# Performance work log

Measured on AMD Instinct MI355X. Metric: run time of the kernel, lower is better.

Reference implementation:

```python
import jax, jax.numpy as jnp
import numpy as np

HIDDEN = 1024
HEADS = 16
N, T1, T2 = 2, 2048, 2048


def setup_inputs() -> dict:
    key = jax.random.key(0)
    k1, k2, k3, k4 = jax.random.split(key, 4)
    q = jax.random.normal(k1, (N, T1, HIDDEN), dtype=jnp.float32)
    encoder_k = jax.random.normal(k2, (N, T2, HIDDEN), dtype=jnp.float32)
    encoder_v = jax.random.normal(k3, (N, T2, HIDDEN), dtype=jnp.float32)
    encoder_attention_mask = jnp.zeros((N, 1, T2, T2), dtype=jnp.float32)
    wo_w = jax.random.normal(k4, (HIDDEN, HIDDEN), dtype=jnp.float32) * (1.0 / np.sqrt(HIDDEN))
    wo_b = jnp.zeros((HIDDEN,), dtype=jnp.float32)
    return {"q": q, "encoder_k": encoder_k, "encoder_v": encoder_v,
            "encoder_attention_mask": encoder_attention_mask,
            "wo_w": wo_w, "wo_b": wo_b}


def _split_heads(x):
    # [N, T, E] -> [N, h, T, d]
    n, t, e = x.shape
    return x.reshape(n, t, HEADS, e // HEADS).transpose(0, 2, 1, 3)


def reference(q, encoder_k, encoder_v, encoder_attention_mask, wo_w, wo_b):
    qh = _split_heads(q)            # [N,h,T1,d]
    kh = _split_heads(encoder_k)    # [N,h,T2,d]
    vh = _split_heads(encoder_v)    # [N,h,T2,d]
    # NOTE: original applies no 1/sqrt(d) scaling
    scores = jnp.einsum('bhqd,bhkd->bhqk', qh, kh) + encoder_attention_mask
    weights = jax.nn.softmax(scores, axis=-1)
    ctx = jnp.einsum('bhqk,bhkd->bhqd', weights, vh)   # [N,h,T1,d]
    ctx = ctx.transpose(0, 2, 1, 3).reshape(q.shape[0], q.shape[1], -1)  # [N,T1,E]
    # wo: Linear (torch: x @ W.T + b) followed by ReLU
    return jax.nn.relu(ctx @ wo_w.T + wo_b)
```

## Files before the change

kernel.cpp:

```cpp
#include <hip/hip_runtime.h>
#include <hip/hip_bf16.h>


typedef short short8 __attribute__((ext_vector_type(8)));
typedef short short4v __attribute__((ext_vector_type(4)));
typedef float floatx4 __attribute__((ext_vector_type(4)));

#define HIDDEN 1024
#define HEADS 16
#define NB 2
#define T1 2048
#define T2 2048

#define LOG2E 1.44269504f
#define SHIFT 28.8539004f
#define VS 68

__device__ __forceinline__ unsigned short f2bf(float f) {
    unsigned u = __float_as_uint(f);
    return (unsigned short)((u + 0x7fffu + ((u >> 16) & 1u)) >> 16);
}

__device__ __forceinline__ short f2bf_native(float f) {
    __hip_bfloat16 h = __float2bfloat16(f);
    return __builtin_bit_cast(short, h);
}

__global__ void zero_kernel(unsigned* f) {
    if (threadIdx.x == 0) *f = 0u;
}

__global__ void prep_kernel(const float4* __restrict__ ek, const float4* __restrict__ ev,
                            const float4* __restrict__ ww, const float4* __restrict__ mask,
                            ushort4* __restrict__ dst, unsigned* __restrict__ flag) {
    const int NK = NB * T2 * HIDDEN / 4;
    const int NW = HIDDEN * HIDDEN / 4;
    if (blockIdx.y == 0) {
        int i = blockIdx.x * blockDim.x + threadIdx.x;
        int stride = gridDim.x * blockDim.x;
        const int n = 2 * NK + NW;
        for (; i < n; i += stride) {
            float4 v = (i < NK) ? ek[i] : (i < 2 * NK) ? ev[i - NK] : ww[i - 2 * NK];
            ushort4 o;
            o.x = f2bf(v.x); o.y = f2bf(v.y); o.z = f2bf(v.z); o.w = f2bf(v.w);
            dst[i] = o;
        }
    } else {
        const int NM = NB * T2 * T2 / 4;
        int i = blockIdx.x * blockDim.x + threadIdx.x;
        int stride = gridDim.x * blockDim.x;
        float mx = 0.f;
        for (; i < NM; i += stride) {
            float4 v = mask[i];
            mx = fmaxf(mx, fmaxf(fmaxf(fabsf(v.x), fabsf(v.y)), fmaxf(fabsf(v.z), fabsf(v.w))));
        }
        for (int d = 32; d; d >>= 1) mx = fmaxf(mx, __shfl_xor(mx, d));
        if ((threadIdx.x & 63) == 0 && mx > 0.f) atomicMax(flag, __float_as_uint(mx));
    }
}

__device__ __forceinline__ void stage_v(short* __restrict__ buf, const short* __restrict__ Vb,
                                        int b, int h, int kc, int tid) {
#pragma unroll
    for (int it = 0; it < 2; ++it) {
        int i = tid + (it << 8);
        int key = i & 63, dg = i >> 6;
        short8 s = *(const short8*)&Vb[(((b * T2) + kc + key) << 10) + (h << 6) + (dg << 3)];
#pragma unroll
        for (int j = 0; j < 8; ++j) buf[(dg * 8 + j) * VS + key] = s[j];
    }
}

__global__ __launch_bounds__(256, 2) void attn_kernel(
        const float* __restrict__ q,
        const short* __restrict__ Kb,
        const short* __restrict__ Vb,
        const float* __restrict__ mask,
        const unsigned* __restrict__ flagp,
        short* __restrict__ ctx)
{
    __shared__ short lV[2][2][64 * VS];

    const int tid = threadIdx.x;
    const int wave = tid >> 6;
    const int lane = tid & 63;
    const int quad = lane >> 4;
    const int l16 = lane & 15;

    const int b = blockIdx.z;
    const int h = blockIdx.y;
    const int q0 = blockIdx.x * 128;

    const bool use_mask = (*flagp != 0u);

    short8 qf[2][2];
#pragma unroll
    for (int rb = 0; rb < 2; ++rb) {
#pragma unroll
        for (int ks = 0; ks < 2; ++ks) {
            const float* qp = q + (((b * T1) + q0 + wave * 32 + rb * 16 + l16) << 10)
                                + (h << 6) + ks * 32 + quad * 8;
            float4 v0 = *(const float4*)qp;
            float4 v1 = *(const float4*)(qp + 4);
            short8 s;
            s[0] = (short)f2bf(v0.x * LOG2E); s[1] = (short)f2bf(v0.y * LOG2E);
            s[2] = (short)f2bf(v0.z * LOG2E); s[3] = (short)f2bf(v0.w * LOG2E);
            s[4] = (short)f2bf(v1.x * LOG2E); s[5] = (short)f2bf(v1.y * LOG2E);
            s[6] = (short)f2bf(v1.z * LOG2E); s[7] = (short)f2bf(v1.w * LOG2E);
            qf[rb][ks] = s;
        }
    }

    floatx4 o_acc[2][4];
#pragma unroll
    for (int rb = 0; rb < 2; ++rb)
#pragma unroll
        for (int cb = 0; cb < 4; ++cb) o_acc[rb][cb] = (floatx4){0.f, 0.f, 0.f, 0.f};
    float l_st[2] = {0.f, 0.f};

    stage_v(lV[0][0], Vb, b, h, 0, tid);
    stage_v(lV[0][1], Vb, b, h, 64, tid);
    short8 kfrag[4][2];
#pragma unroll
    for (int kb = 0; kb < 4; ++kb)
#pragma unroll
        for (int ks = 0; ks < 2; ++ks)
            kfrag[kb][ks] = *(const short8*)
                &Kb[(((b * T2) + kb * 16 + l16) << 10) + (h << 6) + ks * 32 + quad * 8];
    __syncthreads();

    for (int icc = 0; icc < T2 / 128; ++icc) {
        const int kc0 = icc << 7;
        const bool has_next = (icc + 1 < T2 / 128);
        const int kcn = has_next ? kc0 + 128 : kc0;

        short8 vreg[4];
#pragma unroll
        for (int it = 0; it < 4; ++it) {
            int i = tid + ((it & 1) << 8);
            int key = i & 63, dg = i >> 6;
            int half = it >> 1;
            vreg[it] = *(const short8*)
                &Vb[(((b * T2) + kcn + half * 64 + key) << 10) + (h << 6) + (dg << 3)];
        }

        short8 knext[4][2];
#pragma unroll
        for (int kb = 0; kb < 4; ++kb)
#pragma unroll
            for (int ks = 0; ks < 2; ++ks)
                knext[kb][ks] = *(const short8*)
                    &Kb[(((b * T2) + kc0 + 64 + kb * 16 + l16) << 10) + (h << 6) + ks * 32 + quad * 8];

        {
            const short* cur = lV[icc & 1][0];
            const int kc = kc0;
            short4v vfrag[4][4];
#pragma unroll
            for (int kb = 0; kb < 4; ++kb)
#pragma unroll
                for (int cb = 0; cb < 4; ++cb)
                    vfrag[kb][cb] = *(const short4v*)&cur[(cb * 16 + l16) * VS + kb * 16 + quad * 4];

#pragma unroll
            for (int rb = 0; rb < 2; ++rb) {
                floatx4 st[4];
#pragma unroll
                for (int kb = 0; kb < 4; ++kb) {
                    floatx4 a = (floatx4){0.f, 0.f, 0.f, 0.f};
                    a = __builtin_amdgcn_mfma_f32_16x16x32_bf16(kfrag[kb][0], qf[rb][0], a, 0, 0, 0);
                    a = __builtin_amdgcn_mfma_f32_16x16x32_bf16(kfrag[kb][1], qf[rb][1], a, 0, 0, 0);
                    st[kb] = a;
                }
                if (use_mask) {
                    int qrow = q0 + wave * 32 + rb * 16 + l16;
#pragma unroll
                    for (int kb = 0; kb < 4; ++kb)
#pragma unroll
                        for (int r = 0; r < 4; ++r) {
                            int key = kc + kb * 16 + quad * 4 + r;
                            st[kb][r] += mask[(b * T2 + qrow) * T2 + key] * LOG2E;
                        }
                }
                float rs = 0.f;
                short4v pf[4];
#pragma unroll
                for (int kb = 0; kb < 4; ++kb) {
                    float p0 = exp2f(st[kb][0] - SHIFT);
                    float p1 = exp2f(st[kb][1] - SHIFT);
                    float p2 = exp2f(st[kb][2] - SHIFT);
                    float p3 = exp2f(st[kb][3] - SHIFT);
                    rs += (p0 + p1) + (p2 + p3);
                    pf[kb][0] = f2bf_native(p0);
                    pf[kb][1] = f2bf_native(p1);
                    pf[kb][2] = f2bf_native(p2);
                    pf[kb][3] = f2bf_native(p3);
                }
                rs += __shfl_xor(rs, 16);
                rs += __shfl_xor(rs, 32);
                l_st[rb] += rs;

#pragma unroll
                for (int kb = 0; kb < 4; ++kb)
#pragma unroll
                    for (int cb = 0; cb < 4; ++cb)
                        o_acc[rb][cb] = __builtin_amdgcn_mfma_f32_16x16x16bf16_1k(
                            vfrag[kb][cb], pf[kb], o_acc[rb][cb], 0, 0, 0);
            }
        }

#pragma unroll
        for (int kb = 0; kb < 4; ++kb)
#pragma unroll
            for (int ks = 0; ks < 2; ++ks)
                kfrag[kb][ks] = knext[kb][ks];

#pragma unroll
        for (int kb = 0; kb < 4; ++kb)
#pragma unroll
            for (int ks = 0; ks < 2; ++ks)
                knext[kb][ks] = *(const short8*)
                    &Kb[(((b * T2) + kcn + kb * 16 + l16) << 10) + (h << 6) + ks * 32 + quad * 8];

        {
            const short* cur = lV[icc & 1][1];
            const int kc = kc0 + 64;
            short4v vfrag[4][4];
#pragma unroll
            for (int kb = 0; kb < 4; ++kb)
#pragma unroll
                for (int cb = 0; cb < 4; ++cb)
                    vfrag[kb][cb] = *(const short4v*)&cur[(cb * 16 + l16) * VS + kb * 16 + quad * 4];

#pragma unroll
            for (int rb = 0; rb < 2; ++rb) {
                floatx4 st[4];
#pragma unroll
                for (int kb = 0; kb < 4; ++kb) {
                    floatx4 a = (floatx4){0.f, 0.f, 0.f, 0.f};
                    a = __builtin_amdgcn_mfma_f32_16x16x32_bf16(kfrag[kb][0], qf[rb][0], a, 0, 0, 0);
                    a = __builtin_amdgcn_mfma_f32_16x16x32_bf16(kfrag[kb][1], qf[rb][1], a, 0, 0, 0);
                    st[kb] = a;
                }
                if (use_mask) {
                    int qrow = q0 + wave * 32 + rb * 16 + l16;
#pragma unroll
                    for (int kb = 0; kb < 4; ++kb)
#pragma unroll
                        for (int r = 0; r < 4; ++r) {
                            int key = kc + kb * 16 + quad * 4 + r;
                            st[kb][r] += mask[(b * T2 + qrow) * T2 + key] * LOG2E;
                        }
                }
                float rs = 0.f;
                short4v pf[4];
#pragma unroll
                for (int kb = 0; kb < 4; ++kb) {
                    float p0 = exp2f(st[kb][0] - SHIFT);
                    float p1 = exp2f(st[kb][1] - SHIFT);
                    float p2 = exp2f(st[kb][2] - SHIFT);
                    float p3 = exp2f(st[kb][3] - SHIFT);
                    rs += (p0 + p1) + (p2 + p3);
                    pf[kb][0] = f2bf_native(p0);
                    pf[kb][1] = f2bf_native(p1);
                    pf[kb][2] = f2bf_native(p2);
                    pf[kb][3] = f2bf_native(p3);
                }
                rs += __shfl_xor(rs, 16);
                rs += __shfl_xor(rs, 32);
                l_st[rb] += rs;

#pragma unroll
                for (int kb = 0; kb < 4; ++kb)
#pragma unroll
                    for (int cb = 0; cb < 4; ++cb)
                        o_acc[rb][cb] = __builtin_amdgcn_mfma_f32_16x16x16bf16_1k(
                            vfrag[kb][cb], pf[kb], o_acc[rb][cb], 0, 0, 0);
            }
        }

#pragma unroll
        for (int kb = 0; kb < 4; ++kb)
#pragma unroll
            for (int ks = 0; ks < 2; ++ks)
                kfrag[kb][ks] = knext[kb][ks];

        if (has_next) {
#pragma unroll
            for (int it = 0; it < 4; ++it) {
                int i = tid + ((it & 1) << 8);
                int key = i & 63, dg = i >> 6;
                short* nbuf = lV[(icc + 1) & 1][it >> 1];
#pragma unroll
                for (int j = 0; j < 8; ++j) nbuf[(dg * 8 + j) * VS + key] = vreg[it][j];
            }
        }
        __syncthreads();
    }

#pragma unroll
    for (int rb = 0; rb < 2; ++rb) {
        float rinv = 1.0f / l_st[rb];
        int qrow = q0 + wave * 32 + rb * 16 + l16;
#pragma unroll
        for (int cb = 0; cb < 4; ++cb) {
            short4v o;
#pragma unroll
            for (int r = 0; r < 4; ++r) o[r] = (short)f2bf(o_acc[rb][cb][r] * rinv);
            *(short4v*)&ctx[((b * T1 + qrow) << 10) + (h << 6) + cb * 16 + quad * 4] = o;
        }
    }
}

__global__ __launch_bounds__(512) void proj_kernel(
        const short* __restrict__ Cb,
        const short* __restrict__ Wb,
        const float* __restrict__ bias,
        float* __restrict__ out)
{
    __shared__ short lA[2][64 * 72];
    __shared__ short lB[2][128 * 72];

    const int tid = threadIdx.x;
    const int wave = tid >> 6;
    const int lane = tid & 63;
    const int quad = lane >> 4;
    const int l16 = lane & 15;
    const int wm = wave >> 2, wn = wave & 3;
    const int bm = blockIdx.x, bn = blockIdx.y;

    floatx4 acc[2][2];
#pragma unroll
    for (int i = 0; i < 2; ++i)
#pragma unroll
        for (int j = 0; j < 2; ++j) acc[i][j] = (floatx4){0.f, 0.f, 0.f, 0.f};

    short8 ra, rbw[2];
    {
        int row = tid >> 3, c = tid & 7;
        ra = *(const short8*)&Cb[((bm * 64 + row) << 10) + c * 8];
#pragma unroll
        for (int it = 0; it < 2; ++it) {
            int i = tid + it * 512;
            int brow = i >> 3, bc = i & 7;
            rbw[it] = *(const short8*)&Wb[((bn * 128 + brow) << 10) + bc * 8];
        }
    }
    {
        int row = tid >> 3, c = tid & 7;
        *(short8*)&lA[0][row * 72 + c * 8] = ra;
#pragma unroll
        for (int it = 0; it < 2; ++it) {
            int i = tid + it * 512;
            int brow = i >> 3, bc = i & 7;
            *(short8*)&lB[0][brow * 72 + bc * 8] = rbw[it];
        }
    }
    __syncthreads();

    int cur = 0;
    for (int kt = 0; kt < 1024; kt += 64) {
        const bool has_next = (kt + 64 < 1024);
        if (has_next) {
            int row = tid >> 3, c = tid & 7;
            ra = *(const short8*)&Cb[((bm * 64 + row) << 10) + kt + 64 + c * 8];
#pragma unroll
            for (int it = 0; it < 2; ++it) {
                int i = tid + it * 512;
                int brow = i >> 3, bc = i & 7;
                rbw[it] = *(const short8*)&Wb[((bn * 128 + brow) << 10) + kt + 64 + bc * 8];
            }
        }

#pragma unroll
        for (int ks = 0; ks < 2; ++ks) {
            short8 af[2], bf[2];
#pragma unroll
            for (int i = 0; i < 2; ++i)
                af[i] = *(const short8*)&lA[cur][(wm * 32 + i * 16 + l16) * 72 + ks * 32 + quad * 8];
#pragma unroll
            for (int j = 0; j < 2; ++j)
                bf[j] = *(const short8*)&lB[cur][(wn * 32 + j * 16 + l16) * 72 + ks * 32 + quad * 8];
#pragma unroll
            for (int i = 0; i < 2; ++i)
#pragma unroll
                for (int j = 0; j < 2; ++j)
                    acc[i][j] = __builtin_amdgcn_mfma_f32_16x16x32_bf16(af[i], bf[j], acc[i][j], 0, 0, 0);
        }

        if (has_next) {
            int row = tid >> 3, c = tid & 7;
            *(short8*)&lA[cur ^ 1][row * 72 + c * 8] = ra;
#pragma unroll
            for (int it = 0; it < 2; ++it) {
                int i = tid + it * 512;
                int brow = i >> 3, bc = i & 7;
                *(short8*)&lB[cur ^ 1][brow * 72 + bc * 8] = rbw[it];
            }
        }
        __syncthreads();
        cur ^= 1;
    }

    float bv[2];
#pragma unroll
    for (int j = 0; j < 2; ++j) bv[j] = bias[bn * 128 + wn * 32 + j * 16 + l16];

#pragma unroll
    for (int i = 0; i < 2; ++i)
#pragma unroll
        for (int j = 0; j < 2; ++j)
#pragma unroll
            for (int r = 0; r < 4; ++r) {
                int row = bm * 64 + wm * 32 + i * 16 + quad * 4 + r;
                int col = bn * 128 + wn * 32 + j * 16 + l16;
                float v = acc[i][j][r] + bv[j];
                out[(row << 10) + col] = fmaxf(v, 0.f);
            }
}

extern "C" void kernel_launch(void* const* d_in, const int* in_sizes, int n_in,
                              void* d_out, int out_size, void* d_ws, size_t ws_size,
                              hipStream_t stream) {
    const float* q    = (const float*)d_in[0];
    const float* ek   = (const float*)d_in[1];
    const float* ev   = (const float*)d_in[2];
    const float* mask = (const float*)d_in[3];
    const float* wo_w = (const float*)d_in[4];
    const float* wo_b = (const float*)d_in[5];
    float* out = (float*)d_out;

    char* ws = (char*)d_ws;
    unsigned* flag = (unsigned*)ws;
    short* Kb = (short*)(ws + 4096);
    short* Vb = Kb + (NB * T2 * HIDDEN);
    short* Wb = Vb + (NB * T2 * HIDDEN);
    short* Cb = Wb + (HIDDEN * HIDDEN);

    zero_kernel<<<1, 64, 0, stream>>>(flag);
    prep_kernel<<<dim3(512, 2), 256, 0, stream>>>(
        (const float4*)ek, (const float4*)ev, (const float4*)wo_w, (const float4*)mask,
        (ushort4*)Kb, flag);
    attn_kernel<<<dim3(T1 / 128, HEADS, NB), 256, 0, stream>>>(q, Kb, Vb, mask, flag, Cb);
    proj_kernel<<<dim3(64, 8), 512, 0, stream>>>(Cb, Wb, wo_b, out);
}
```

Measured before the change: 233.8 us.

## Split attention across two KV halves with a separate combine kernel

Adds a split-KV attention kernel in which each block handles half of the key sequence. Each block writes fp32 partial outputs and row sums, and a new combine kernel sums the two halves and normalizes. This doubles the grid from 512 to 1024 blocks to fill the CUs better, and it is safe because the softmax uses a fixed shift rather than a running max. The cost is extra fp32 partial traffic, an additional launch, and a larger workspace. The fallback kernel is also reworked to a single 64-key LDS stage per iteration.

```diff
diff --git a/kernel.cpp b/kernel.cpp
--- a/kernel.cpp
+++ b/kernel.cpp
@@ -71,15 +71,16 @@
     }
 }
 
-__global__ __launch_bounds__(256, 2) void attn_kernel(
+__global__ __launch_bounds__(256, 2) void attn_split_kernel(
         const float* __restrict__ q,
         const short* __restrict__ Kb,
         const short* __restrict__ Vb,
         const float* __restrict__ mask,
         const unsigned* __restrict__ flagp,
-        short* __restrict__ ctx)
+        float* __restrict__ Opart,
+        float* __restrict__ lpart)
 {
-    __shared__ short lV[2][2][64 * VS];
+    __shared__ short lV[2][64 * VS];
 
     const int tid = threadIdx.x;
     const int wave = tid >> 6;
@@ -89,7 +90,11 @@
 
     const int b = blockIdx.z;
     const int h = blockIdx.y;
-    const int q0 = blockIdx.x * 128;
+    const int qb = blockIdx.x >> 1;
+    const int half = blockIdx.x & 1;
+    const int q0 = qb * 128;
+    const int kv0 = half * (T2 / 2);
+    const int NC = (T2 / 2) / 64;
 
     const bool use_mask = (*flagp != 0u);
 
@@ -118,8 +123,188 @@
         for (int cb = 0; cb < 4; ++cb) o_acc[rb][cb] = (floatx4){0.f, 0.f, 0.f, 0.f};
     float l_st[2] = {0.f, 0.f};
 
-    stage_v(lV[0][0], Vb, b, h, 0, tid);
-    stage_v(lV[0][1], Vb, b, h, 64, tid);
+    stage_v(lV[0], Vb, b, h, kv0, tid);
+    short8 kfrag[4][2];
+#pragma unroll
+    for (int kb = 0; kb < 4; ++kb)
+#pragma unroll
+        for (int ks = 0; ks < 2; ++ks)
+            kfrag[kb][ks] = *(const short8*)
+                &Kb[(((b * T2) + kv0 + kb * 16 + l16) << 10) + (h << 6) + ks * 32 + quad * 8];
+    __syncthreads();
+
+    for (int ic = 0; ic < NC; ++ic) {
+        const int kc = kv0 + (ic << 6);
+        const short* cur = lV[ic & 1];
+        const bool has_next = (ic + 1 < NC);
+        const int kcn = has_next ? kc + 64 : kc;
+
+        short8 vreg[2];
+#pragma unroll
+        for (int it = 0; it < 2; ++it) {
+            int i = tid + (it << 8);
+            int key = i & 63, dg = i >> 6;
+            vreg[it] = *(const short8*)&Vb[(((b * T2) + kcn + key) << 10) + (h << 6) + (dg << 3)];
+        }
+
+        short8 knext[4][2];
+#pragma unroll
+        for (int kb = 0; kb < 4; ++kb)
+#pragma unroll
+            for (int ks = 0; ks < 2; ++ks)
+                knext[kb][ks] = *(const short8*)
+                    &Kb[(((b * T2) + kcn + kb * 16 + l16) << 10) + (h << 6) + ks * 32 + quad * 8];
+
+        short4v vfrag[4][4];
+#pragma unroll
+        for (int kb = 0; kb < 4; ++kb)
+#pragma unroll
+            for (int cb = 0; cb < 4; ++cb)
+                vfrag[kb][cb] = *(const short4v*)&cur[(cb * 16 + l16) * VS + kb * 16 + quad * 4];
+
+#pragma unroll
+        for (int rb = 0; rb < 2; ++rb) {
+            floatx4 st[4];
+#pragma unroll
+            for (int kb = 0; kb < 4; ++kb) {
+                floatx4 a = (floatx4){0.f, 0.f, 0.f, 0.f};
+                a = __builtin_amdgcn_mfma_f32_16x16x32_bf16(kfrag[kb][0], qf[rb][0], a, 0, 0, 0);
+                a = __builtin_amdgcn_mfma_f32_16x16x32_bf16(kfrag[kb][1], qf[rb][1], a, 0, 0, 0);
+                st[kb] = a;
+            }
+            if (use_mask) {
+                int qrow = q0 + wave * 32 + rb * 16 + l16;
+#pragma unroll
+                for (int kb = 0; kb < 4; ++kb)
+#pragma unroll
+                    for (int r = 0; r < 4; ++r) {
+                        int key = kc + kb * 16 + quad * 4 + r;
+                        st[kb][r] += mask[(b * T2 + qrow) * T2 + key] * LOG2E;
+                    }
+            }
+            float rs = 0.f;
+            short4v pf[4];
+#pragma unroll
+            for (int kb = 0; kb < 4; ++kb) {
+                float p0 = exp2f(st[kb][0] - SHIFT);
+                float p1 = exp2f(st[kb][1] - SHIFT);
+                float p2 = exp2f(st[kb][2] - SHIFT);
+                float p3 = exp2f(st[kb][3] - SHIFT);
+                rs += (p0 + p1) + (p2 + p3);
+                pf[kb][0] = f2bf_native(p0);
+                pf[kb][1] = f2bf_native(p1);
+                pf[kb][2] = f2bf_native(p2);
+                pf[kb][3] = f2bf_native(p3);
+            }
+            rs += __shfl_xor(rs, 16);
+            rs += __shfl_xor(rs, 32);
+            l_st[rb] += rs;
+
+#pragma unroll
+            for (int kb = 0; kb < 4; ++kb)
+#pragma unroll
+                for (int cb = 0; cb < 4; ++cb)
+                    o_acc[rb][cb] = __builtin_amdgcn_mfma_f32_16x16x16bf16_1k(
+                        vfrag[kb][cb], pf[kb], o_acc[rb][cb], 0, 0, 0);
+        }
+
+        if (has_next) {
+            short* nbuf = lV[(ic + 1) & 1];
+#pragma unroll
+            for (int it = 0; it < 2; ++it) {
+                int i = tid + (it << 8);
+                int key = i & 63, dg = i >> 6;
+#pragma unroll
+                for (int j = 0; j < 8; ++j) nbuf[(dg * 8 + j) * VS + key] = vreg[it][j];
+            }
+        }
+
+#pragma unroll
+        for (int kb = 0; kb < 4; ++kb)
+#pragma unroll
+            for (int ks = 0; ks < 2; ++ks)
+                kfrag[kb][ks] = knext[kb][ks];
+
+        __syncthreads();
+    }
+
+    float* Op = Opart + half * (NB * T1 * HIDDEN);
+    float* lp = lpart + half * (NB * T1 * HEADS);
+#pragma unroll
+    for (int rb = 0; rb < 2; ++rb) {
+        float l = l_st[rb];
+        int qrow = q0 + wave * 32 + rb * 16 + l16;
+        if (quad == 0) lp[(b * T1 + qrow) * HEADS + h] = l;
+#pragma unroll
+        for (int cb = 0; cb < 4; ++cb)
+            *(floatx4*)&Op[((b * T1 + qrow) << 10) + (h << 6) + cb * 16 + quad * 4] = o_acc[rb][cb];
+    }
+}
+
+__global__ __launch_bounds__(256) void combine_kernel(
+        const float* __restrict__ Opart, const float* __restrict__ lpart,
+        short* __restrict__ ctx) {
+    int idx = blockIdx.x * blockDim.x + threadIdx.x;
+    int e = idx << 2;
+    int row = e >> 10;
+    int h = (e & 1023) >> 6;
+    floatx4 a = *(const floatx4*)&Opart[e];
+    floatx4 c = *(const floatx4*)&Opart[NB * T1 * HIDDEN + e];
+    float l = lpart[row * HEADS + h] + lpart[NB * T1 * HEADS + row * HEADS + h];
+    float rinv = 1.0f / l;
+    short4v o;
+#pragma unroll
+    for (int j = 0; j < 4; ++j) o[j] = (short)f2bf((a[j] + c[j]) * rinv);
+    *(short4v*)&ctx[e] = o;
+}
+
+__global__ __launch_bounds__(256, 2) void attn_kernel(
+        const float* __restrict__ q,
+        const short* __restrict__ Kb,
+        const short* __restrict__ Vb,
+        const float* __restrict__ mask,
+        const unsigned* __restrict__ flagp,
+        short* __restrict__ ctx) {
+    __shared__ short lV[2][64 * VS];
+
+    const int tid = threadIdx.x;
+    const int wave = tid >> 6;
+    const int lane = tid & 63;
+    const int quad = lane >> 4;
+    const int l16 = lane & 15;
+
+    const int b = blockIdx.z;
+    const int h = blockIdx.y;
+    const int q0 = blockIdx.x * 128;
+
+    const bool use_mask = (*flagp != 0u);
+
+    short8 qf[2][2];
+#pragma unroll
+    for (int rb = 0; rb < 2; ++rb) {
+#pragma unroll
+        for (int ks = 0; ks < 2; ++ks) {
+            const float* qp = q + (((b * T1) + q0 + wave * 32 + rb * 16 + l16) << 10)
+                                + (h << 6) + ks * 32 + quad * 8;
+            float4 v0 = *(const float4*)qp;
+            float4 v1 = *(const float4*)(qp + 4);
+            short8 s;
+            s[0] = (short)f2bf(v0.x * LOG2E); s[1] = (short)f2bf(v0.y * LOG2E);
+            s[2] = (short)f2bf(v0.z * LOG2E); s[3] = (short)f2bf(v0.w * LOG2E);
+            s[4] = (short)f2bf(v1.x * LOG2E); s[5] = (short)f2bf(v1.y * LOG2E);
+            s[6] = (short)f2bf(v1.z * LOG2E); s[7] = (short)f2bf(v1.w * LOG2E);
+            qf[rb][ks] = s;
+        }
+    }
+
+    floatx4 o_acc[2][4];
+#pragma unroll
+    for (int rb = 0; rb < 2; ++rb)
+#pragma unroll
+        for (int cb = 0; cb < 4; ++cb) o_acc[rb][cb] = (floatx4){0.f, 0.f, 0.f, 0.f};
+    float l_st[2] = {0.f, 0.f};
+
+    stage_v(lV[0], Vb, b, h, 0, tid);
     short8 kfrag[4][2];
 #pragma unroll
     for (int kb = 0; kb < 4; ++kb)
@@ -129,92 +314,21 @@
                 &Kb[(((b * T2) + kb * 16 + l16) << 10) + (h << 6) + ks * 32 + quad * 8];
     __syncthreads();
 
-    for (int icc = 0; icc < T2 / 128; ++icc) {
-        const int kc0 = icc << 7;
-        const bool has_next = (icc + 1 < T2 / 128);
-        const int kcn = has_next ? kc0 + 128 : kc0;
-
-        short8 vreg[4];
-#pragma unroll
-        for (int it = 0; it < 4; ++it) {
-            int i = tid + ((it & 1) << 8);
+    for (int ic = 0; ic < T2 / 64; ++ic) {
+        const int kc = ic << 6;
+        const short* cur = lV[ic & 1];
+        const bool has_next = (ic + 1 < T2 / 64);
+        const int kcn = has_next ? kc + 64 : kc;
+
+        short8 vreg[2];
+#pragma unroll
+        for (int it = 0; it < 2; ++it) {
+            int i = tid + (it << 8);
             int key = i & 63, dg = i >> 6;
-            int half = it >> 1;
-            vreg[it] = *(const short8*)
-                &Vb[(((b * T2) + kcn + half * 64 + key) << 10) + (h << 6) + (dg << 3)];
+            vreg[it] = *(const short8*)&Vb[(((b * T2) + kcn + key) << 10) + (h << 6) + (dg << 3)];
         }
 
         short8 knext[4][2];
-#pragma unroll
-        for (int kb = 0; kb < 4; ++kb)
-#pragma unroll
-            for (int ks = 0; ks < 2; ++ks)
-                knext[kb][ks] = *(const short8*)
-                    &Kb[(((b * T2) + kc0 + 64 + kb * 16 + l16) << 10) + (h << 6) + ks * 32 + quad * 8];
-
-        {
-            const short* cur = lV[icc & 1][0];
-            const int kc = kc0;
-            short4v vfrag[4][4];
-#pragma unroll
-            for (int kb = 0; kb < 4; ++kb)
-#pragma unroll
-                for (int cb = 0; cb < 4; ++cb)
-                    vfrag[kb][cb] = *(const short4v*)&cur[(cb * 16 + l16) * VS + kb * 16 + quad * 4];
-
-#pragma unroll
-            for (int rb = 0; rb < 2; ++rb) {
-                floatx4 st[4];
-#pragma unroll
-                for (int kb = 0; kb < 4; ++kb) {
-                    floatx4 a = (floatx4){0.f, 0.f, 0.f, 0.f};
-                    a = __builtin_amdgcn_mfma_f32_16x16x32_bf16(kfrag[kb][0], qf[rb][0], a, 0, 0, 0);
-                    a = __builtin_amdgcn_mfma_f32_16x16x32_bf16(kfrag[kb][1], qf[rb][1], a, 0, 0, 0);
-                    st[kb] = a;
-                }
-                if (use_mask) {
-                    int qrow = q0 + wave * 32 + rb * 16 + l16;
-#pragma unroll
-                    for (int kb = 0; kb < 4; ++kb)
-#pragma unroll
-                        for (int r = 0; r < 4; ++r) {
-                            int key = kc + kb * 16 + quad * 4 + r;
-                            st[kb][r] += mask[(b * T2 + qrow) * T2 + key] * LOG2E;
-                        }
-                }
-                float rs = 0.f;
-                short4v pf[4];
-#pragma unroll
-                for (int kb = 0; kb < 4; ++kb) {
-                    float p0 = exp2f(st[kb][0] - SHIFT);
-                    float p1 = exp2f(st[kb][1] - SHIFT);
-                    float p2 = exp2f(st[kb][2] - SHIFT);
-                    float p3 = exp2f(st[kb][3] - SHIFT);
-                    rs += (p0 + p1) + (p2 + p3);
-                    pf[kb][0] = f2bf_native(p0);
-                    pf[kb][1] = f2bf_native(p1);
-                    pf[kb][2] = f2bf_native(p2);
-                    pf[kb][3] = f2bf_native(p3);
-                }
-                rs += __shfl_xor(rs, 16);
-                rs += __shfl_xor(rs, 32);
-                l_st[rb] += rs;
-
-#pragma unroll
-                for (int kb = 0; kb < 4; ++kb)
-#pragma unroll
-                    for (int cb = 0; cb < 4; ++cb)
-                        o_acc[rb][cb] = __builtin_amdgcn_mfma_f32_16x16x16bf16_1k(
-                            vfrag[kb][cb], pf[kb], o_acc[rb][cb], 0, 0, 0);
-            }
-        }
-
-#pragma unroll
-        for (int kb = 0; kb < 4; ++kb)
-#pragma unroll
-            for (int ks = 0; ks < 2; ++ks)
-                kfrag[kb][ks] = knext[kb][ks];
-
 #pragma unroll
         for (int kb = 0; kb < 4; ++kb)
 #pragma unroll
@@ -222,60 +336,67 @@
                 knext[kb][ks] = *(const short8*)
                     &Kb[(((b * T2) + kcn + kb * 16 + l16) << 10) + (h << 6) + ks * 32 + quad * 8];
 
-        {
-            const short* cur = lV[icc & 1][1];
-            const int kc = kc0 + 64;
-            short4v vfrag[4][4];
+        short4v vfrag[4][4];
+#pragma unroll
+        for (int kb = 0; kb < 4; ++kb)
+#pragma unroll
+            for (int cb = 0; cb < 4; ++cb)
+                vfrag[kb][cb] = *(const short4v*)&cur[(cb * 16 + l16) * VS + kb * 16 + quad * 4];
+
+#pragma unroll
+        for (int rb = 0; rb < 2; ++rb) {
+            floatx4 st[4];
+#pragma unroll
+            for (int kb = 0; kb < 4; ++kb) {
+                floatx4 a = (floatx4){0.f, 0.f, 0.f, 0.f};
+                a = __builtin_amdgcn_mfma_f32_16x16x32_bf16(kfrag[kb][0], qf[rb][0], a, 0, 0, 0);
+                a = __builtin_amdgcn_mfma_f32_16x16x32_bf16(kfrag[kb][1], qf[rb][1], a, 0, 0, 0);
+                st[kb] = a;
+            }
+            if (use_mask) {
+                int qrow = q0 + wave * 32 + rb * 16 + l16;
+#pragma unroll
+                for (int kb = 0; kb < 4; ++kb)
+#pragma unroll
+                    for (int r = 0; r < 4; ++r) {
+                        int key = kc + kb * 16 + quad * 4 + r;
+                        st[kb][r] += mask[(b * T2 + qrow) * T2 + key] * LOG2E;
+                    }
+            }
+            float rs = 0.f;
+            short4v pf[4];
+#pragma unroll
+            for (int kb = 0; kb < 4; ++kb) {
+                float p0 = exp2f(st[kb][0] - SHIFT);
+                float p1 = exp2f(st[kb][1] - SHIFT);
+                float p2 = exp2f(st[kb][2] - SHIFT);
+                float p3 = exp2f(st[kb][3] - SHIFT);
+                rs += (p0 + p1) + (p2 + p3);
+                pf[kb][0] = f2bf_native(p0);
+                pf[kb][1] = f2bf_native(p1);
+                pf[kb][2] = f2bf_native(p2);
+                pf[kb][3] = f2bf_native(p3);
+            }
+            rs += __shfl_xor(rs, 16);
+            rs += __shfl_xor(rs, 32);
+            l_st[rb] += rs;
+
 #pragma unroll
             for (int kb = 0; kb < 4; ++kb)
 #pragma unroll
                 for (int cb = 0; cb < 4; ++cb)
-                    vfrag[kb][cb] = *(const short4v*)&cur[(cb * 16 + l16) * VS + kb * 16 + quad * 4];
-
-#pragma unroll
-            for (int rb = 0; rb < 2; ++rb) {
-                floatx4 st[4];
-#pragma unroll
-                for (int kb = 0; kb < 4; ++kb) {
-                    floatx4 a = (floatx4){0.f, 0.f, 0.f, 0.f};
-                    a = __builtin_amdgcn_mfma_f32_16x16x32_bf16(kfrag[kb][0], qf[rb][0], a, 0, 0, 0);
-                    a = __builtin_amdgcn_mfma_f32_16x16x32_bf16(kfrag[kb][1], qf[rb][1], a, 0, 0, 0);
-                    st[kb] = a;
-                }
-                if (use_mask) {
-                    int qrow = q0 + wave * 32 + rb * 16 + l16;
-#pragma unroll
-                    for (int kb = 0; kb < 4; ++kb)
-#pragma unroll
-                        for (int r = 0; r < 4; ++r) {
-                            int key = kc + kb * 16 + quad * 4 + r;
-                            st[kb][r] += mask[(b * T2 + qrow) * T2 + key] * LOG2E;
-                        }
-                }
-                float rs = 0.f;
-                short4v pf[4];
-#pragma unroll
-                for (int kb = 0; kb < 4; ++kb) {
-                    float p0 = exp2f(st[kb][0] - SHIFT);
-                    float p1 = exp2f(st[kb][1] - SHIFT);
-                    float p2 = exp2f(st[kb][2] - SHIFT);
-                    float p3 = exp2f(st[kb][3] - SHIFT);
-                    rs += (p0 + p1) + (p2 + p3);
-                    pf[kb][0] = f2bf_native(p0);
-                    pf[kb][1] = f2bf_native(p1);
-                    pf[kb][2] = f2bf_native(p2);
-                    pf[kb][3] = f2bf_native(p3);
-                }
-                rs += __shfl_xor(rs, 16);
-                rs += __shfl_xor(rs, 32);
-                l_st[rb] += rs;
-
-#pragma unroll
-                for (int kb = 0; kb < 4; ++kb)
-#pragma unroll
-                    for (int cb = 0; cb < 4; ++cb)
-                        o_acc[rb][cb] = __builtin_amdgcn_mfma_f32_16x16x16bf16_1k(
-                            vfrag[kb][cb], pf[kb], o_acc[rb][cb], 0, 0, 0);
+                    o_acc[rb][cb] = __builtin_amdgcn_mfma_f32_16x16x16bf16_1k(
+                        vfrag[kb][cb], pf[kb], o_acc[rb][cb], 0, 0, 0);
+        }
+
+        if (has_next) {
+            short* nbuf = lV[(ic + 1) & 1];
+#pragma unroll
+            for (int it = 0; it < 2; ++it) {
+                int i = tid + (it << 8);
+                int key = i & 63, dg = i >> 6;
+#pragma unroll
+                for (int j = 0; j < 8; ++j) nbuf[(dg * 8 + j) * VS + key] = vreg[it][j];
             }
         }
 
@@ -285,16 +406,6 @@
             for (int ks = 0; ks < 2; ++ks)
                 kfrag[kb][ks] = knext[kb][ks];
 
-        if (has_next) {
-#pragma unroll
-            for (int it = 0; it < 4; ++it) {
-                int i = tid + ((it & 1) << 8);
-                int key = i & 63, dg = i >> 6;
-                short* nbuf = lV[(icc + 1) & 1][it >> 1];
-#pragma unroll
-                for (int j = 0; j < 8; ++j) nbuf[(dg * 8 + j) * VS + key] = vreg[it][j];
-            }
-        }
         __syncthreads();
     }
 
@@ -436,11 +547,23 @@
     short* Vb = Kb + (NB * T2 * HIDDEN);
     short* Wb = Vb + (NB * T2 * HIDDEN);
     short* Cb = Wb + (HIDDEN * HIDDEN);
+    const size_t base = 4096 + (size_t)(NB * T2 * HIDDEN) * 4 + (size_t)HIDDEN * HIDDEN * 2
+                      + (size_t)NB * T1 * HIDDEN * 2;
+    float* Opart = (float*)(ws + base);
+    float* lpart = (float*)(ws + base + (size_t)2 * NB * T1 * HIDDEN * 4);
+    const size_t need = base + (size_t)2 * NB * T1 * HIDDEN * 4
+                      + (size_t)2 * NB * T1 * HEADS * 4;
 
     zero_kernel<<<1, 64, 0, stream>>>(flag);
     prep_kernel<<<dim3(512, 2), 256, 0, stream>>>(
         (const float4*)ek, (const float4*)ev, (const float4*)wo_w, (const float4*)mask,
         (ushort4*)Kb, flag);
-    attn_kernel<<<dim3(T1 / 128, HEADS, NB), 256, 0, stream>>>(q, Kb, Vb, mask, flag, Cb);
+    if (ws_size >= need) {
+        attn_split_kernel<<<dim3(T1 / 128 * 2, HEADS, NB), 256, 0, stream>>>(
+            q, Kb, Vb, mask, flag, Opart, lpart);
+        combine_kernel<<<NB * T1 * HIDDEN / 4 / 256, 256, 0, stream>>>(Opart, lpart, Cb);
+    } else {
+        attn_kernel<<<dim3(T1 / 128, HEADS, NB), 256, 0, stream>>>(q, Kb, Vb, mask, flag, Cb);
+    }
     proj_kernel<<<dim3(64, 8), 512, 0, stream>>>(Cb, Wb, wo_b, out);
 }
```

Measured after the change: 236.5 us. About the same (+1.2%).
